# Kernel optimization log

Measured on AMD Instinct MI355X. Metric: run time of the kernel, lower is better.

The kernel has to match this reference:

```python
import jax, jax.numpy as jnp
import numpy as np

B, M, H = 4, 128, 1024      # docs, padded mentions per doc, LUKE-large hidden
NH, L = 16, 1024            # attention heads, seq_len
E = 64                      # padded entities per doc
R = 512                     # entity pairs per doc
EMB, BS, NC = 768, 64, 97   # embed_size, block_size, num_class


def setup_inputs() -> dict:
    key = jax.random.key(0)
    ks = jax.random.split(key, 12)
    inp = {
        "seq_lhs": jax.random.normal(ks[0], (B, L, H), jnp.float32),
        "ent_lhs": jax.random.normal(ks[1], (B, M, H), jnp.float32),
        "ent_to_seq_attn": jax.random.uniform(ks[2], (B, NH, M, L), jnp.float32),
        "entity_id_labels": jax.random.randint(ks[3], (B, M), 0, E),
        "hts": jax.random.randint(ks[4], (B, R, 2), 0, E),
        "Wh": jax.random.normal(ks[5], (2 * H, EMB), jnp.float32) * 0.02,
        "bh": jax.random.normal(ks[6], (EMB,), jnp.float32) * 0.02,
        "Wt": jax.random.normal(ks[7], (2 * H, EMB), jnp.float32) * 0.02,
        "bt": jax.random.normal(ks[8], (EMB,), jnp.float32) * 0.02,
        "Wb": jax.random.normal(ks[9], (EMB * BS, NC), jnp.float32) * 0.02,
        "bb": jax.random.normal(ks[10], (NC,), jnp.float32) * 0.02,
    }
    return inp


def reference(seq_lhs, ent_lhs, ent_to_seq_attn, entity_id_labels, hts,
              Wh, bh, Wt, bt, Wb, bb):
    # ---- mention -> entity pooling (segment logsumexp / segment mean) ----
    # global segment id per mention: doc_i * E + entity_label
    ids = (jnp.arange(B)[:, None] * E + entity_id_labels).reshape(-1)  # [B*M]
    m = ent_lhs.reshape(B * M, H)

    seg_max = jax.ops.segment_max(m, ids, num_segments=B * E)          # [B*E, H]
    seg_max = jnp.where(jnp.isfinite(seg_max), seg_max, 0.0)           # empty -> 0
    sumexp = jax.ops.segment_sum(jnp.exp(m - seg_max[ids]), ids, num_segments=B * E)
    cnt = jax.ops.segment_sum(jnp.ones((B * M,), m.dtype), ids, num_segments=B * E)  # [B*E]
    lse = seg_max + jnp.log(jnp.maximum(sumexp, 1e-30))
    ent_embeds = jnp.where(cnt[:, None] > 0, lse, 0.0).reshape(B, E, H)

    # mean of entity-to-seq attention over mentions of each entity
    a = ent_to_seq_attn.transpose(0, 2, 1, 3).reshape(B * M, NH, L)
    a_sum = jax.ops.segment_sum(a, ids, num_segments=B * E)            # [B*E, NH, L]
    ent_attn = (a_sum / jnp.maximum(cnt, 1.0)[:, None, None]).reshape(B, E, NH, L)

    # ---- gather head/tail entities for each pair ----
    h_idx, t_idx = hts[..., 0], hts[..., 1]                            # [B, R]
    hs = jnp.take_along_axis(ent_embeds, h_idx[..., None], axis=1)     # [B, R, H]
    ts = jnp.take_along_axis(ent_embeds, t_idx[..., None], axis=1)
    h_attn = jnp.take_along_axis(ent_attn, h_idx[..., None, None], axis=1)  # [B, R, NH, L]
    t_attn = jnp.take_along_axis(ent_attn, t_idx[..., None, None], axis=1)

    # ---- attn-weighted relation-context embedding ----
    ht_attn = (h_attn * t_attn).mean(axis=2)                           # [B, R, L]
    ht_attn = ht_attn / (ht_attn.sum(-1, keepdims=True) + 1e-5)
    rel = jnp.einsum('bld,brl->brd', seq_lhs, ht_attn)                 # [B, R, H]

    # ---- extractors + block bilinear classifier ----
    hs = jnp.tanh(jnp.concatenate([hs, rel], -1) @ Wh + bh)            # [B, R, EMB]
    ts = jnp.tanh(jnp.concatenate([ts, rel], -1) @ Wt + bt)
    N, K = B * R, EMB // BS
    b1 = hs.reshape(N, K, BS)
    b2 = ts.reshape(N, K, BS)
    bl = (b1[:, :, :, None] * b2[:, :, None, :]).reshape(N, EMB * BS)  # [N, 49152]
    class_logits = bl @ Wb + bb                                        # [N, NC]
    return class_logits
```

## Files before the change

### kernel.cpp

```cpp
#include <hip/hip_runtime.h>
#include <cmath>

#define B_ 4
#define M_ 128
#define H_ 1024
#define NH_ 16
#define L_ 1024
#define E_ 64
#define R_ 512
#define EMB_ 768
#define BS_ 64
#define NC_ 97
#define NPAIR_ (B_*R_)
#define LC_ 16

typedef _Float16 half8 __attribute__((ext_vector_type(8)));
typedef float f32x4 __attribute__((ext_vector_type(4)));

#define OFF_ENT    0
#define OFF_ATTNH  262144
#define OFF_VH     2359296
#define OFF_S      3407872
#define OFF_SEQT   3409920
#define OFF_RELH   5507072
#define OFF_HSF    6555648
#define OFF_TSF    7342080
#define OFF_WHT    8128512
#define OFF_WTT    8914944

__device__ __forceinline__ void gload_lds16(const void* g, void* l) {
    __builtin_amdgcn_global_load_lds(
        (const __attribute__((address_space(1))) unsigned int*)g,
        (__attribute__((address_space(3))) unsigned int*)l, 16, 0, 0);
}

__global__ __launch_bounds__(256) void k_ent_pool(const float* __restrict__ ent_lhs,
                                                  const int* __restrict__ labels,
                                                  float* __restrict__ ent_embeds) {
    int blk = blockIdx.x;
    int b = blk >> 6, e = blk & 63;
    __shared__ int lbl[M_];
    int t = threadIdx.x;
    if (t < M_) lbl[t] = labels[b*M_ + t];
    __syncthreads();
    const float* src = ent_lhs + (size_t)b * M_ * H_;
    float mx[4], sm[4];
    #pragma unroll
    for (int j = 0; j < 4; ++j) { mx[j] = -INFINITY; sm[j] = 0.f; }
    int cnt = 0;
    for (int m = 0; m < M_; ++m) {
        if (lbl[m] != e) continue;
        ++cnt;
        const float* row = src + m * H_;
        #pragma unroll
        for (int j = 0; j < 4; ++j) {
            float x = row[t + j*256];
            if (x > mx[j]) { sm[j] = sm[j] * __expf(mx[j] - x) + 1.f; mx[j] = x; }
            else           { sm[j] += __expf(x - mx[j]); }
        }
    }
    float* dst = ent_embeds + (size_t)blk * H_;
    #pragma unroll
    for (int j = 0; j < 4; ++j)
        dst[t + j*256] = (cnt > 0) ? (mx[j] + __logf(sm[j])) : 0.f;
}

__global__ __launch_bounds__(256) void k_ent_attn(const float* __restrict__ attn,
                                                  const int* __restrict__ labels,
                                                  _Float16* __restrict__ ea_t) {
    int blk = blockIdx.x;
    int b = blk >> 6, e = blk & 63;
    __shared__ int lbl[M_];
    int t = threadIdx.x;
    if (t < M_) lbl[t] = labels[b*M_ + t];
    __syncthreads();
    const float* src = attn + (size_t)b * NH_ * M_ * L_;
    float acc[16][4] = {};
    int cnt = 0;
    for (int m = 0; m < M_; ++m) {
        if (lbl[m] != e) continue;
        ++cnt;
        const float* mp = src + (size_t)m * L_ + t*4;
        #pragma unroll
        for (int nh = 0; nh < 16; ++nh) {
            float4 v = *(const float4*)(mp + (size_t)nh * M_ * L_);
            acc[nh][0] += v.x; acc[nh][1] += v.y; acc[nh][2] += v.z; acc[nh][3] += v.w;
        }
    }
    float inv = 1.f / fmaxf((float)cnt, 1.f);
    _Float16* dst = ea_t + (size_t)blk * L_ * 16;
    #pragma unroll
    for (int j = 0; j < 4; ++j) {
        int l = t*4 + j;
        half8 o0, o1;
        #pragma unroll
        for (int nh = 0; nh < 8; ++nh) { o0[nh] = (_Float16)(acc[nh][j]*inv); o1[nh] = (_Float16)(acc[nh+8][j]*inv); }
        *(half8*)(dst + (size_t)l*16)     = o0;
        *(half8*)(dst + (size_t)l*16 + 8) = o1;
    }
}

__global__ __launch_bounds__(256) void k_ht(const _Float16* __restrict__ ea_t,
                                            const int* __restrict__ hts,
                                            _Float16* __restrict__ vh) {
    int blk = blockIdx.x;
    int b = blk >> 6, lc = blk & 63;
    int l0 = lc * LC_;
    __shared__ _Float16 tile[64*256];
    int t = threadIdx.x;
    {
        int e = t >> 2, part = t & 3;
        const _Float16* src = ea_t + ((size_t)(b*64 + e)*L_ + l0) * 16;
        #pragma unroll
        for (int u = 0; u < 8; ++u) {
            int unit = part*8 + u;
            int l = unit >> 1, nhh = unit & 1;
            half8 v = *(const half8*)(src + l*16 + nhh*8);
            *(half8*)&tile[e*256 + ((l ^ (e & 15))*16) + nhh*8] = v;
        }
    }
    __syncthreads();
    const int* hp = hts + b * R_ * 2;
    #pragma unroll
    for (int pp = 0; pp < 2; ++pp) {
        int p = pp*256 + t;
        int he = hp[p*2], te = hp[p*2 + 1];
        const _Float16* ha = &tile[he*256];
        const _Float16* ta = &tile[te*256];
        float accl[LC_];
        #pragma unroll
        for (int l = 0; l < LC_; ++l) {
            half8 h0 = *(const half8*)&ha[((l ^ (he & 15))*16)];
            half8 h1 = *(const half8*)&ha[((l ^ (he & 15))*16) + 8];
            half8 t0 = *(const half8*)&ta[((l ^ (te & 15))*16)];
            half8 t1 = *(const half8*)&ta[((l ^ (te & 15))*16) + 8];
            float s = 0.f;
            #pragma unroll
            for (int q = 0; q < 8; ++q)
                s += (float)h0[q]*(float)t0[q] + (float)h1[q]*(float)t1[q];
            accl[l] = s;
        }
        half8 o0, o1;
        #pragma unroll
        for (int q = 0; q < 8; ++q) { o0[q] = (_Float16)accl[q]; o1[q] = (_Float16)accl[q+8]; }
        _Float16* dst = vh + (size_t)(b*R_ + p)*L_ + l0;
        *(half8*)dst = o0;
        *(half8*)(dst + 8) = o1;
    }
}

__global__ __launch_bounds__(256) void k_rowsum(const _Float16* __restrict__ vh,
                                                float* __restrict__ s) {
    int row = blockIdx.x*4 + (threadIdx.x >> 6);
    int lane = threadIdx.x & 63;
    const _Float16* r = vh + (size_t)row * L_;
    float acc = 0.f;
    #pragma unroll
    for (int u = 0; u < 2; ++u) {
        half8 v = *(const half8*)(r + (lane + u*64)*8);
        #pragma unroll
        for (int q = 0; q < 8; ++q) acc += (float)v[q];
    }
    #pragma unroll
    for (int off = 32; off > 0; off >>= 1) acc += __shfl_down(acc, off);
    if (lane == 0) s[row] = acc;
}

__global__ __launch_bounds__(256) void k_prep_seqt(const float* __restrict__ seq,
                                                   _Float16* __restrict__ seqT) {
    int l0 = blockIdx.x*64, d0 = blockIdx.y*64, b = blockIdx.z;
    __shared__ _Float16 sl[64*72];
    int t = threadIdx.x;
    int lr = t >> 4, dc = (t & 15)*4;
    #pragma unroll
    for (int u = 0; u < 4; ++u) {
        int l = lr + u*16;
        float4 v = *(const float4*)(seq + ((size_t)(b*L_ + l0 + l))*H_ + d0 + dc);
        sl[l*72 + dc+0] = (_Float16)v.x; sl[l*72 + dc+1] = (_Float16)v.y;
        sl[l*72 + dc+2] = (_Float16)v.z; sl[l*72 + dc+3] = (_Float16)v.w;
    }
    __syncthreads();
    int d = t >> 2, lo = (t & 3)*16;
    half8 o0, o1;
    #pragma unroll
    for (int q = 0; q < 8; ++q) { o0[q] = sl[(lo+q)*72 + d]; o1[q] = sl[(lo+8+q)*72 + d]; }
    _Float16* dst = seqT + ((size_t)(b*H_ + d0 + d))*L_ + l0 + lo;
    *(half8*)dst = o0;
    *(half8*)(dst + 8) = o1;
}

__global__ __launch_bounds__(256) void k_prep_wt(const float* __restrict__ W,
                                                 _Float16* __restrict__ WT) {
    int k0 = blockIdx.x * 64;
    int d0 = blockIdx.y * 64;
    __shared__ float s[64*65];
    int t = threadIdx.x;
    #pragma unroll
    for (int u = 0; u < 16; ++u) {
        int idx = t + u*256; int rr = idx >> 6, cc = idx & 63;
        s[rr*65 + cc] = W[(size_t)(k0+rr)*EMB_ + d0 + cc];
    }
    __syncthreads();
    #pragma unroll
    for (int u = 0; u < 16; ++u) {
        int idx = t + u*256; int dd = idx >> 6, kk = idx & 63;
        WT[(size_t)(d0+dd)*2048 + k0 + kk] = (_Float16)s[kk*65 + dd];
    }
}

__global__ __launch_bounds__(256) void k_prep_wbt(const float* __restrict__ Wb,
                                                  _Float16* __restrict__ Wbt) {
    int kbi = blockIdx.x;
    __shared__ float s[64*97];
    int t = threadIdx.x;
    size_t gbase = (size_t)kbi * 64 * NC_;
    #pragma unroll
    for (int u = 0; u < 25; ++u) {
        int idx = t + u*256;
        if (idx < 64*NC_) s[idx] = Wb[gbase + idx];
    }
    __syncthreads();
    _Float16* dst = Wbt + (size_t)kbi * 8192;
    #pragma unroll
    for (int u = 0; u < 32; ++u) {
        int idx = t + u*256;
        int c = idx >> 6, j = idx & 63;
        float v = (c < NC_) ? s[j*NC_ + c] : 0.f;
        dst[idx] = (_Float16)v;
    }
}

__global__ __launch_bounds__(256) void k_rel_mfma(const _Float16* __restrict__ vh,
                                                  const _Float16* __restrict__ seqT,
                                                  const float* __restrict__ s,
                                                  _Float16* __restrict__ relh) {
    const int d0 = blockIdx.x * 64;
    const int n0 = blockIdx.y * 64;
    const int b  = n0 >> 9;
    __shared__ _Float16 bs[2][64*64];
    const int t = threadIdx.x;
    const int w = t >> 6, lane = t & 63;
    const int r = lane & 15, g = lane >> 4;
    const int row8 = lane >> 3, u8 = lane & 7;
    const int swz_w = (u8 ^ row8) * 8;

    const _Float16* bsrc = seqT + ((size_t)(b*H_) + d0) * L_;
    #pragma unroll
    for (int c2 = w*2; c2 < w*2+2; ++c2)
        gload_lds16(bsrc + (size_t)(c2*8 + row8)*L_ + swz_w, &bs[0][c2*512]);

    const _Float16* ap = vh + (size_t)(n0 + w*16 + r) * L_;
    half8 nA0 = *(const half8*)(ap + g*8);
    half8 nA1 = *(const half8*)(ap + 32 + g*8);

    f32x4 acc[4] = {};
    __syncthreads();

    for (int c = 0; c < 16; ++c) {
        const int cur = c & 1;
        if (c < 15) {
            const int k0n = (c+1)*64;
            #pragma unroll
            for (int c2 = w*2; c2 < w*2+2; ++c2)
                gload_lds16(bsrc + (size_t)(c2*8 + row8)*L_ + k0n + swz_w, &bs[cur^1][c2*512]);
        }
        half8 cA0 = nA0, cA1 = nA1;
        if (c < 15) {
            const int k0n = (c+1)*64;
            nA0 = *(const half8*)(ap + k0n + g*8);
            nA1 = *(const half8*)(ap + k0n + 32 + g*8);
        }
        #pragma unroll
        for (int df = 0; df < 4; ++df) {
            half8 b0 = *(const half8*)&bs[cur][(df*16 + r)*64 + ((g ^ (r&7))*8)];
            acc[df] = __builtin_amdgcn_mfma_f32_16x16x32_f16(cA0, b0, acc[df], 0, 0, 0);
            half8 b1 = *(const half8*)&bs[cur][(df*16 + r)*64 + (((4+g) ^ (r&7))*8)];
            acc[df] = __builtin_amdgcn_mfma_f32_16x16x32_f16(cA1, b1, acc[df], 0, 0, 0);
        }
        __syncthreads();
    }
    const int nb = n0 + w*16 + g*4;
    float invs[4];
    #pragma unroll
    for (int q = 0; q < 4; ++q) invs[q] = 1.f / (s[nb + q] + 1.6e-4f);
    #pragma unroll
    for (int df = 0; df < 4; ++df)
        #pragma unroll
        for (int q = 0; q < 4; ++q)
            relh[(size_t)(nb + q)*H_ + d0 + df*16 + r] = (_Float16)(acc[df][q] * invs[q]);
}

__global__ __launch_bounds__(256) void k_extract_mfma(const float* __restrict__ ent_embeds,
                                                      const _Float16* __restrict__ relh,
                                                      const int* __restrict__ hts,
                                                      const _Float16* __restrict__ WhT,
                                                      const _Float16* __restrict__ WtT,
                                                      const float* __restrict__ bh,
                                                      const float* __restrict__ bt,
                                                      _Float16* __restrict__ hsf,
                                                      _Float16* __restrict__ tsf) {
    const int which = blockIdx.z;
    const _Float16* WT = which ? WtT : WhT;
    const float* bias  = which ? bt : bh;
    _Float16* outh     = which ? tsf : hsf;

    const int d0 = blockIdx.x * 64;
    const int n0 = blockIdx.y * 64;
    __shared__ _Float16 wt_s[2][64*64];
    const int t = threadIdx.x;
    const int w = t >> 6, lane = t & 63;
    const int r = lane & 15, g = lane >> 4;
    const int row8 = lane >> 3, u8 = lane & 7;
    const int swz_w = (u8 ^ row8) * 8;

    const int nrow = n0 + w*16 + r;
    const int hidx = hts[nrow*2 + which];
    const float* entp = ent_embeds + ((size_t)((nrow >> 9)*E_ + hidx))*H_;
    const _Float16* relp = relh + (size_t)nrow * H_;

    #pragma unroll
    for (int c2 = w*2; c2 < w*2+2; ++c2)
        gload_lds16(WT + (size_t)(d0 + c2*8 + row8)*2048 + swz_w, &wt_s[0][c2*512]);

    float4 nF0 = *(const float4*)(entp + g*8);
    float4 nF1 = *(const float4*)(entp + g*8 + 4);
    float4 nF2 = *(const float4*)(entp + 32 + g*8);
    float4 nF3 = *(const float4*)(entp + 32 + g*8 + 4);
    half8 nH0 = {}, nH1 = {};

    f32x4 acc[4] = {};
    __syncthreads();

    for (int c = 0; c < 32; ++c) {
        const int cur = c & 1;
        if (c < 31) {
            const int k0n = (c+1)*64;
            #pragma unroll
            for (int c2 = w*2; c2 < w*2+2; ++c2)
                gload_lds16(WT + (size_t)(d0 + c2*8 + row8)*2048 + k0n + swz_w,
                            &wt_s[cur^1][c2*512]);
        }
        half8 aF0, aF1;
        if (c < 16) {
            aF0 = half8{ (_Float16)nF0.x, (_Float16)nF0.y, (_Float16)nF0.z, (_Float16)nF0.w,
                         (_Float16)nF1.x, (_Float16)nF1.y, (_Float16)nF1.z, (_Float16)nF1.w };
            aF1 = half8{ (_Float16)nF2.x, (_Float16)nF2.y, (_Float16)nF2.z, (_Float16)nF2.w,
                         (_Float16)nF3.x, (_Float16)nF3.y, (_Float16)nF3.z, (_Float16)nF3.w };
        } else {
            aF0 = nH0; aF1 = nH1;
        }
        if (c < 31) {
            const int k0n = (c+1)*64;
            if (k0n < 1024) {
                const float* ar = entp + k0n;
                nF0 = *(const float4*)(ar + g*8);
                nF1 = *(const float4*)(ar + g*8 + 4);
                nF2 = *(const float4*)(ar + 32 + g*8);
                nF3 = *(const float4*)(ar + 32 + g*8 + 4);
            } else {
                const _Float16* ar = relp + (k0n - 1024);
                nH0 = *(const half8*)(ar + g*8);
                nH1 = *(const half8*)(ar + 32 + g*8);
            }
        }
        #pragma unroll
        for (int df = 0; df < 4; ++df) {
            half8 b0 = *(const half8*)&wt_s[cur][(df*16 + r)*64 + ((g ^ (r&7))*8)];
            acc[df] = __builtin_amdgcn_mfma_f32_16x16x32_f16(aF0, b0, acc[df], 0, 0, 0);
            half8 b1 = *(const half8*)&wt_s[cur][(df*16 + r)*64 + (((4+g) ^ (r&7))*8)];
            acc[df] = __builtin_amdgcn_mfma_f32_16x16x32_f16(aF1, b1, acc[df], 0, 0, 0);
        }
        __syncthreads();
    }
    #pragma unroll
    for (int df = 0; df < 4; ++df) {
        float bv = bias[d0 + df*16 + r];
        #pragma unroll
        for (int q2 = 0; q2 < 4; ++q2) {
            float v = tanhf(acc[df][q2] + bv);
            outh[(size_t)(n0 + w*16 + g*4 + q2)*EMB_ + d0 + df*16 + r] = (_Float16)v;
        }
    }
}

__global__ __launch_bounds__(256) void k_cls_mfma(const _Float16* __restrict__ hsf,
                                                  const _Float16* __restrict__ tsf,
                                                  const _Float16* __restrict__ Wbt,
                                                  float* __restrict__ partial) {
    const int kb = blockIdx.x;
    const int n0 = blockIdx.y * 128;
    const int t = threadIdx.x;
    const int w = t >> 6, lane = t & 63;
    const int r = lane & 15, g = lane >> 4;
    __shared__ _Float16 hs_s[128*72];

    {
        int n = t & 127, hh = t >> 7;
        const _Float16* src = &hsf[(size_t)(n0+n)*EMB_ + kb*64 + hh*32];
        #pragma unroll
        for (int u = 0; u < 4; ++u)
            *(half8*)&hs_s[n*72 + hh*32 + u*8] = *(const half8*)(src + u*8);
    }
    half8 tsF[8][2];
    #pragma unroll
    for (int nf = 0; nf < 8; ++nf) {
        const _Float16* tp = &tsf[(size_t)(n0 + nf*16 + r)*EMB_ + kb*64];
        tsF[nf][0] = *(const half8*)(tp + g*8);
        tsF[nf][1] = *(const half8*)(tp + 32 + g*8);
    }
    __syncthreads();

    const _Float16* wb = Wbt + (size_t)(kb*64) * 8192;
    f32x4 acc[8][2] = {};

    #pragma unroll 2
    for (int i = 0; i < 64; ++i) {
        const _Float16* ws_ = wb + (size_t)i * 8192;
        half8 b00, b01, b10, b11;
        {
            const _Float16* bp0 = ws_ + (size_t)(w*32 + r)*64;
            const _Float16* bp1 = ws_ + (size_t)(w*32 + 16 + r)*64;
            b00 = *(const half8*)(bp0 + g*8);
            b01 = *(const half8*)(bp0 + 32 + g*8);
            b10 = *(const half8*)(bp1 + g*8);
            b11 = *(const half8*)(bp1 + 32 + g*8);
        }
        #pragma unroll
        for (int nf = 0; nf < 8; ++nf) {
            _Float16 h = hs_s[(nf*16 + r)*72 + i];
            half8 a0, a1;
            #pragma unroll
            for (int e = 0; e < 8; ++e) { a0[e] = tsF[nf][0][e] * h; a1[e] = tsF[nf][1][e] * h; }
            acc[nf][0] = __builtin_amdgcn_mfma_f32_16x16x32_f16(a0, b00, acc[nf][0], 0, 0, 0);
            acc[nf][0] = __builtin_amdgcn_mfma_f32_16x16x32_f16(a1, b01, acc[nf][0], 0, 0, 0);
            acc[nf][1] = __builtin_amdgcn_mfma_f32_16x16x32_f16(a0, b10, acc[nf][1], 0, 0, 0);
            acc[nf][1] = __builtin_amdgcn_mfma_f32_16x16x32_f16(a1, b11, acc[nf][1], 0, 0, 0);
        }
    }
    float* pdst = partial + (size_t)kb * 2048 * 128;
    #pragma unroll
    for (int nf = 0; nf < 8; ++nf) {
        #pragma unroll
        for (int cl = 0; cl < 2; ++cl) {
            int c = w*32 + cl*16 + r;
            #pragma unroll
            for (int q = 0; q < 4; ++q)
                pdst[(size_t)(n0 + nf*16 + g*4 + q)*128 + c] = acc[nf][cl][q];
        }
    }
}

__global__ __launch_bounds__(256) void k_reduce(const float* __restrict__ partial,
                                                const float* __restrict__ bb,
                                                float* __restrict__ out) {
    int idx = blockIdx.x*256 + threadIdx.x;
    if (idx >= NPAIR_*NC_) return;
    int n = idx / NC_, c = idx - n*NC_;
    float s = bb[c];
    #pragma unroll
    for (int kb = 0; kb < 12; ++kb)
        s += partial[((size_t)kb*2048 + n)*128 + c];
    out[idx] = s;
}

extern "C" void kernel_launch(void* const* d_in, const int* in_sizes, int n_in,
                              void* d_out, int out_size, void* d_ws, size_t ws_size,
                              hipStream_t stream) {
    (void)in_sizes; (void)n_in; (void)out_size; (void)ws_size;
    const float* seq  = (const float*)d_in[0];
    const float* ent  = (const float*)d_in[1];
    const float* attn = (const float*)d_in[2];
    const int*   lbl  = (const int*)d_in[3];
    const int*   hts  = (const int*)d_in[4];
    const float* Wh   = (const float*)d_in[5];
    const float* bh   = (const float*)d_in[6];
    const float* Wt   = (const float*)d_in[7];
    const float* bt   = (const float*)d_in[8];
    const float* Wb   = (const float*)d_in[9];
    const float* bb   = (const float*)d_in[10];
    float* out = (float*)d_out;
    float* ws  = (float*)d_ws;

    float*    ent_embeds = ws + OFF_ENT;
    _Float16* ea_t = (_Float16*)(ws + OFF_ATTNH);
    _Float16* vh   = (_Float16*)(ws + OFF_VH);
    float*    sv   = ws + OFF_S;
    _Float16* seqT = (_Float16*)(ws + OFF_SEQT);
    _Float16* relh = (_Float16*)(ws + OFF_RELH);
    _Float16* hsf  = (_Float16*)(ws + OFF_HSF);
    _Float16* tsf  = (_Float16*)(ws + OFF_TSF);
    _Float16* WhT  = (_Float16*)(ws + OFF_WHT);
    _Float16* WtT  = (_Float16*)(ws + OFF_WTT);
    _Float16* Wbt  = (_Float16*)(ws + OFF_ATTNH);
    float*    part = ws + OFF_SEQT;

    k_prep_seqt<<<dim3(16, 16, 4), 256, 0, stream>>>(seq, seqT);
    k_prep_wt<<<dim3(32, 12), 256, 0, stream>>>(Wh, WhT);
    k_prep_wt<<<dim3(32, 12), 256, 0, stream>>>(Wt, WtT);
    k_ent_pool<<<B_*E_, 256, 0, stream>>>(ent, lbl, ent_embeds);
    k_ent_attn<<<B_*E_, 256, 0, stream>>>(attn, lbl, ea_t);
    k_ht<<<B_*64, 256, 0, stream>>>(ea_t, hts, vh);
    k_rowsum<<<NPAIR_/4, 256, 0, stream>>>(vh, sv);
    k_rel_mfma<<<dim3(16, 32), 256, 0, stream>>>(vh, seqT, sv, relh);
    k_prep_wbt<<<768, 256, 0, stream>>>(Wb, Wbt);
    k_extract_mfma<<<dim3(12, 32, 2), 256, 0, stream>>>(ent_embeds, relh, hts, WhT, WtT, bh, bt, hsf, tsf);
    k_cls_mfma<<<dim3(12, 16), 256, 0, stream>>>(hsf, tsf, Wbt, part);
    k_reduce<<<(NPAIR_*NC_ + 255)/256, 256, 0, stream>>>(part, bb, out);
}
```

Measured before the change: 292.6 us.

## Split extractor GEMM into per-entity and per-pair parts and enlarge MFMA tiles

The concat([ent, rel]) @ W product is split algebraically. The entity half is computed once per unique entity (256 rows) instead of once per pair, and the relation half is computed per pair. Both halves for Wh and Wt go through one larger 128x128-tile MFMA GEMM into an fp16 buffer G. A small combine kernel then gathers by hts, adds the bias and applies tanh. The rel GEMM also moves to 128x64 tiles with both operands staged in LDS, and the workspace layout is reshuffled. This removes redundant FLOPs on the entity half, at the cost of an extra fp16 rounding of partial sums and one extra kernel launch.

Result: faster. 281.2 us (-3.9%).

```diff
diff --git a/kernel.cpp b/kernel.cpp
--- a/kernel.cpp
+++ b/kernel.cpp
@@ -17,16 +17,17 @@
 typedef _Float16 half8 __attribute__((ext_vector_type(8)));
 typedef float f32x4 __attribute__((ext_vector_type(4)));
 
-#define OFF_ENT    0
-#define OFF_ATTNH  262144
-#define OFF_VH     2359296
-#define OFF_S      3407872
-#define OFF_SEQT   3409920
-#define OFF_RELH   5507072
-#define OFF_HSF    6555648
-#define OFF_TSF    7342080
-#define OFF_WHT    8128512
-#define OFF_WTT    8914944
+#define OFF_EAT    0
+#define OFF_VH     2097152
+#define OFF_PART   0
+#define OFF_SEQT   3145728
+#define OFF_G      3145728
+#define OFF_RELH   5242880
+#define OFF_WBT    6291456
+#define OFF_ENTH   9437184
+#define OFF_SV     9568256
+#define OFF_WHT    9570304
+#define OFF_WTT    10356736
 
 __device__ __forceinline__ void gload_lds16(const void* g, void* l) {
     __builtin_amdgcn_global_load_lds(
@@ -36,7 +37,7 @@
 
 __global__ __launch_bounds__(256) void k_ent_pool(const float* __restrict__ ent_lhs,
                                                   const int* __restrict__ labels,
-                                                  float* __restrict__ ent_embeds) {
+                                                  _Float16* __restrict__ enth) {
     int blk = blockIdx.x;
     int b = blk >> 6, e = blk & 63;
     __shared__ int lbl[M_];
@@ -59,10 +60,10 @@
             else           { sm[j] += __expf(x - mx[j]); }
         }
     }
-    float* dst = ent_embeds + (size_t)blk * H_;
+    _Float16* dst = enth + (size_t)blk * H_;
     #pragma unroll
     for (int j = 0; j < 4; ++j)
-        dst[t + j*256] = (cnt > 0) ? (mx[j] + __logf(sm[j])) : 0.f;
+        dst[t + j*256] = (_Float16)((cnt > 0) ? (mx[j] + __logf(sm[j])) : 0.f);
 }
 
 __global__ __launch_bounds__(256) void k_ent_attn(const float* __restrict__ attn,
@@ -230,157 +231,181 @@
     }
 }
 
-__global__ __launch_bounds__(256) void k_rel_mfma(const _Float16* __restrict__ vh,
-                                                  const _Float16* __restrict__ seqT,
-                                                  const float* __restrict__ s,
-                                                  _Float16* __restrict__ relh) {
-    const int d0 = blockIdx.x * 64;
-    const int n0 = blockIdx.y * 64;
-    const int b  = n0 >> 9;
-    __shared__ _Float16 bs[2][64*64];
+__global__ __launch_bounds__(256) void k_relmm(const _Float16* __restrict__ vh,
+                                               const _Float16* __restrict__ seqT,
+                                               const float* __restrict__ sv,
+                                               _Float16* __restrict__ relh) {
+    const int nt = blockIdx.x;
+    const int mt = blockIdx.y;
+    const int b  = mt >> 2;
+    __shared__ _Float16 As[2][128*64];
+    __shared__ _Float16 Bs[2][64*64];
     const int t = threadIdx.x;
     const int w = t >> 6, lane = t & 63;
     const int r = lane & 15, g = lane >> 4;
-    const int row8 = lane >> 3, u8 = lane & 7;
-    const int swz_w = (u8 ^ row8) * 8;
-
-    const _Float16* bsrc = seqT + ((size_t)(b*H_) + d0) * L_;
-    #pragma unroll
-    for (int c2 = w*2; c2 < w*2+2; ++c2)
-        gload_lds16(bsrc + (size_t)(c2*8 + row8)*L_ + swz_w, &bs[0][c2*512]);
-
-    const _Float16* ap = vh + (size_t)(n0 + w*16 + r) * L_;
-    half8 nA0 = *(const half8*)(ap + g*8);
-    half8 nA1 = *(const half8*)(ap + 32 + g*8);
-
-    f32x4 acc[4] = {};
-    __syncthreads();
-
-    for (int c = 0; c < 16; ++c) {
-        const int cur = c & 1;
-        if (c < 15) {
-            const int k0n = (c+1)*64;
-            #pragma unroll
-            for (int c2 = w*2; c2 < w*2+2; ++c2)
-                gload_lds16(bsrc + (size_t)(c2*8 + row8)*L_ + k0n + swz_w, &bs[cur^1][c2*512]);
-        }
-        half8 cA0 = nA0, cA1 = nA1;
-        if (c < 15) {
-            const int k0n = (c+1)*64;
-            nA0 = *(const half8*)(ap + k0n + g*8);
-            nA1 = *(const half8*)(ap + k0n + 32 + g*8);
-        }
-        #pragma unroll
-        for (int df = 0; df < 4; ++df) {
-            half8 b0 = *(const half8*)&bs[cur][(df*16 + r)*64 + ((g ^ (r&7))*8)];
-            acc[df] = __builtin_amdgcn_mfma_f32_16x16x32_f16(cA0, b0, acc[df], 0, 0, 0);
-            half8 b1 = *(const half8*)&bs[cur][(df*16 + r)*64 + (((4+g) ^ (r&7))*8)];
-            acc[df] = __builtin_amdgcn_mfma_f32_16x16x32_f16(cA1, b1, acc[df], 0, 0, 0);
-        }
+    const int wm = w >> 1, wn = w & 1;
+    const int srow = lane >> 3, scol = ((lane & 7) ^ srow) * 8;
+
+    const _Float16* Ab = vh + (size_t)mt*128*1024;
+    const _Float16* Bb = seqT + ((size_t)b*1024 + nt*64)*1024;
+
+    #pragma unroll
+    for (int cc = 0; cc < 6; ++cc) {
+        int c = w*6 + cc;
+        if (c < 16) gload_lds16(Ab + (size_t)(c*8 + srow)*1024 + scol, &As[0][c*512]);
+        else        gload_lds16(Bb + (size_t)((c-16)*8 + srow)*1024 + scol, &Bs[0][(c-16)*512]);
+    }
+    f32x4 acc[4][2] = {};
+    __syncthreads();
+
+    for (int k = 0; k < 16; ++k) {
+        const int cur = k & 1;
+        if (k < 15) {
+            const int k0 = (k+1)*64;
+            #pragma unroll
+            for (int cc = 0; cc < 6; ++cc) {
+                int c = w*6 + cc;
+                if (c < 16) gload_lds16(Ab + (size_t)(c*8 + srow)*1024 + k0 + scol, &As[cur^1][c*512]);
+                else        gload_lds16(Bb + (size_t)((c-16)*8 + srow)*1024 + k0 + scol, &Bs[cur^1][(c-16)*512]);
+            }
+        }
+        half8 aF[4][2], bF[2][2];
+        #pragma unroll
+        for (int mf = 0; mf < 4; ++mf) {
+            int row = wm*64 + mf*16 + r;
+            aF[mf][0] = *(const half8*)&As[cur][row*64 + ((g ^ (r&7))*8)];
+            aF[mf][1] = *(const half8*)&As[cur][row*64 + (((4+g) ^ (r&7))*8)];
+        }
+        #pragma unroll
+        for (int nf = 0; nf < 2; ++nf) {
+            int row = wn*32 + nf*16 + r;
+            bF[nf][0] = *(const half8*)&Bs[cur][row*64 + ((g ^ (r&7))*8)];
+            bF[nf][1] = *(const half8*)&Bs[cur][row*64 + (((4+g) ^ (r&7))*8)];
+        }
+        #pragma unroll
+        for (int mf = 0; mf < 4; ++mf)
+            #pragma unroll
+            for (int nf = 0; nf < 2; ++nf) {
+                acc[mf][nf] = __builtin_amdgcn_mfma_f32_16x16x32_f16(aF[mf][0], bF[nf][0], acc[mf][nf], 0, 0, 0);
+                acc[mf][nf] = __builtin_amdgcn_mfma_f32_16x16x32_f16(aF[mf][1], bF[nf][1], acc[mf][nf], 0, 0, 0);
+            }
         __syncthreads();
     }
-    const int nb = n0 + w*16 + g*4;
-    float invs[4];
-    #pragma unroll
-    for (int q = 0; q < 4; ++q) invs[q] = 1.f / (s[nb + q] + 1.6e-4f);
-    #pragma unroll
-    for (int df = 0; df < 4; ++df)
-        #pragma unroll
-        for (int q = 0; q < 4; ++q)
-            relh[(size_t)(nb + q)*H_ + d0 + df*16 + r] = (_Float16)(acc[df][q] * invs[q]);
-}
-
-__global__ __launch_bounds__(256) void k_extract_mfma(const float* __restrict__ ent_embeds,
-                                                      const _Float16* __restrict__ relh,
-                                                      const int* __restrict__ hts,
-                                                      const _Float16* __restrict__ WhT,
-                                                      const _Float16* __restrict__ WtT,
-                                                      const float* __restrict__ bh,
-                                                      const float* __restrict__ bt,
-                                                      _Float16* __restrict__ hsf,
-                                                      _Float16* __restrict__ tsf) {
-    const int which = blockIdx.z;
-    const _Float16* WT = which ? WtT : WhT;
-    const float* bias  = which ? bt : bh;
-    _Float16* outh     = which ? tsf : hsf;
-
-    const int d0 = blockIdx.x * 64;
-    const int n0 = blockIdx.y * 64;
-    __shared__ _Float16 wt_s[2][64*64];
+    #pragma unroll
+    for (int mf = 0; mf < 4; ++mf) {
+        int nb = mt*128 + wm*64 + mf*16 + g*4;
+        float invs[4];
+        #pragma unroll
+        for (int q = 0; q < 4; ++q) invs[q] = 1.f / (sv[nb + q] + 1.6e-4f);
+        #pragma unroll
+        for (int nf = 0; nf < 2; ++nf) {
+            int d = nt*64 + wn*32 + nf*16 + r;
+            #pragma unroll
+            for (int q = 0; q < 4; ++q)
+                relh[(size_t)(nb + q)*1024 + d] = (_Float16)(acc[mf][nf][q] * invs[q]);
+        }
+    }
+}
+
+__global__ __launch_bounds__(256) void k_bigmm(const _Float16* __restrict__ relh,
+                                               const _Float16* __restrict__ enth,
+                                               const _Float16* __restrict__ WhT,
+                                               const _Float16* __restrict__ WtT,
+                                               _Float16* __restrict__ G) {
+    const int nt = blockIdx.x;
+    const int mt = blockIdx.y;
+    __shared__ _Float16 As[2][128*64];
+    __shared__ _Float16 Bs[2][128*64];
     const int t = threadIdx.x;
     const int w = t >> 6, lane = t & 63;
     const int r = lane & 15, g = lane >> 4;
-    const int row8 = lane >> 3, u8 = lane & 7;
-    const int swz_w = (u8 ^ row8) * 8;
-
-    const int nrow = n0 + w*16 + r;
-    const int hidx = hts[nrow*2 + which];
-    const float* entp = ent_embeds + ((size_t)((nrow >> 9)*E_ + hidx))*H_;
-    const _Float16* relp = relh + (size_t)nrow * H_;
-
-    #pragma unroll
-    for (int c2 = w*2; c2 < w*2+2; ++c2)
-        gload_lds16(WT + (size_t)(d0 + c2*8 + row8)*2048 + swz_w, &wt_s[0][c2*512]);
-
-    float4 nF0 = *(const float4*)(entp + g*8);
-    float4 nF1 = *(const float4*)(entp + g*8 + 4);
-    float4 nF2 = *(const float4*)(entp + 32 + g*8);
-    float4 nF3 = *(const float4*)(entp + 32 + g*8 + 4);
-    half8 nH0 = {}, nH1 = {};
-
-    f32x4 acc[4] = {};
-    __syncthreads();
-
-    for (int c = 0; c < 32; ++c) {
-        const int cur = c & 1;
-        if (c < 31) {
-            const int k0n = (c+1)*64;
-            #pragma unroll
-            for (int c2 = w*2; c2 < w*2+2; ++c2)
-                gload_lds16(WT + (size_t)(d0 + c2*8 + row8)*2048 + k0n + swz_w,
-                            &wt_s[cur^1][c2*512]);
-        }
-        half8 aF0, aF1;
-        if (c < 16) {
-            aF0 = half8{ (_Float16)nF0.x, (_Float16)nF0.y, (_Float16)nF0.z, (_Float16)nF0.w,
-                         (_Float16)nF1.x, (_Float16)nF1.y, (_Float16)nF1.z, (_Float16)nF1.w };
-            aF1 = half8{ (_Float16)nF2.x, (_Float16)nF2.y, (_Float16)nF2.z, (_Float16)nF2.w,
-                         (_Float16)nF3.x, (_Float16)nF3.y, (_Float16)nF3.z, (_Float16)nF3.w };
-        } else {
-            aF0 = nH0; aF1 = nH1;
-        }
-        if (c < 31) {
-            const int k0n = (c+1)*64;
-            if (k0n < 1024) {
-                const float* ar = entp + k0n;
-                nF0 = *(const float4*)(ar + g*8);
-                nF1 = *(const float4*)(ar + g*8 + 4);
-                nF2 = *(const float4*)(ar + 32 + g*8);
-                nF3 = *(const float4*)(ar + 32 + g*8 + 4);
-            } else {
-                const _Float16* ar = relp + (k0n - 1024);
-                nH0 = *(const half8*)(ar + g*8);
-                nH1 = *(const half8*)(ar + 32 + g*8);
+    const int wm = w >> 1, wn = w & 1;
+    const int srow = lane >> 3, scol = ((lane & 7) ^ srow) * 8;
+
+    const _Float16* Ab = (mt < 16) ? (relh + (size_t)mt*128*1024)
+                                   : (enth + (size_t)(mt-16)*128*1024);
+    const int koff = (mt < 16) ? 1024 : 0;
+    const _Float16* Bb = ((nt < 6) ? (WhT + (size_t)nt*128*2048)
+                                   : (WtT + (size_t)(nt-6)*128*2048)) + koff;
+
+    #pragma unroll
+    for (int cc = 0; cc < 4; ++cc) {
+        int c = w*4 + cc;
+        gload_lds16(Ab + (size_t)(c*8 + srow)*1024 + scol, &As[0][c*512]);
+        gload_lds16(Bb + (size_t)(c*8 + srow)*2048 + scol, &Bs[0][c*512]);
+    }
+    f32x4 acc[4][4] = {};
+    __syncthreads();
+
+    for (int k = 0; k < 16; ++k) {
+        const int cur = k & 1;
+        if (k < 15) {
+            const int k0 = (k+1)*64;
+            #pragma unroll
+            for (int cc = 0; cc < 4; ++cc) {
+                int c = w*4 + cc;
+                gload_lds16(Ab + (size_t)(c*8 + srow)*1024 + k0 + scol, &As[cur^1][c*512]);
+                gload_lds16(Bb + (size_t)(c*8 + srow)*2048 + k0 + scol, &Bs[cur^1][c*512]);
             }
         }
-        #pragma unroll
-        for (int df = 0; df < 4; ++df) {
-            half8 b0 = *(const half8*)&wt_s[cur][(df*16 + r)*64 + ((g ^ (r&7))*8)];
-            acc[df] = __builtin_amdgcn_mfma_f32_16x16x32_f16(aF0, b0, acc[df], 0, 0, 0);
-            half8 b1 = *(const half8*)&wt_s[cur][(df*16 + r)*64 + (((4+g) ^ (r&7))*8)];
-            acc[df] = __builtin_amdgcn_mfma_f32_16x16x32_f16(aF1, b1, acc[df], 0, 0, 0);
-        }
+        half8 aF[4][2], bF[4][2];
+        #pragma unroll
+        for (int mf = 0; mf < 4; ++mf) {
+            int row = wm*64 + mf*16 + r;
+            aF[mf][0] = *(const half8*)&As[cur][row*64 + ((g ^ (r&7))*8)];
+            aF[mf][1] = *(const half8*)&As[cur][row*64 + (((4+g) ^ (r&7))*8)];
+        }
+        #pragma unroll
+        for (int nf = 0; nf < 4; ++nf) {
+            int row = wn*64 + nf*16 + r;
+            bF[nf][0] = *(const half8*)&Bs[cur][row*64 + ((g ^ (r&7))*8)];
+            bF[nf][1] = *(const half8*)&Bs[cur][row*64 + (((4+g) ^ (r&7))*8)];
+        }
+        #pragma unroll
+        for (int mf = 0; mf < 4; ++mf)
+            #pragma unroll
+            for (int nf = 0; nf < 4; ++nf) {
+                acc[mf][nf] = __builtin_amdgcn_mfma_f32_16x16x32_f16(aF[mf][0], bF[nf][0], acc[mf][nf], 0, 0, 0);
+                acc[mf][nf] = __builtin_amdgcn_mfma_f32_16x16x32_f16(aF[mf][1], bF[nf][1], acc[mf][nf], 0, 0, 0);
+            }
         __syncthreads();
     }
     #pragma unroll
-    for (int df = 0; df < 4; ++df) {
-        float bv = bias[d0 + df*16 + r];
-        #pragma unroll
-        for (int q2 = 0; q2 < 4; ++q2) {
-            float v = tanhf(acc[df][q2] + bv);
-            outh[(size_t)(n0 + w*16 + g*4 + q2)*EMB_ + d0 + df*16 + r] = (_Float16)v;
-        }
-    }
+    for (int mf = 0; mf < 4; ++mf) {
+        int nrow = mt*128 + wm*64 + mf*16 + g*4;
+        #pragma unroll
+        for (int nf = 0; nf < 4; ++nf) {
+            int v = nt*128 + wn*64 + nf*16 + r;
+            #pragma unroll
+            for (int q = 0; q < 4; ++q)
+                G[(size_t)(nrow + q)*1536 + v] = (_Float16)acc[mf][nf][q];
+        }
+    }
+}
+
+__global__ __launch_bounds__(192) void k_combine(const _Float16* __restrict__ G,
+                                                 const int* __restrict__ hts,
+                                                 const float* __restrict__ bh,
+                                                 const float* __restrict__ bt,
+                                                 _Float16* __restrict__ hsf,
+                                                 _Float16* __restrict__ tsf) {
+    int n = blockIdx.x;
+    int b = n >> 9;
+    int t = threadIdx.x;
+    int side = t / 96, u = t % 96;
+    int d0 = u*8;
+    int idx = hts[n*2 + side];
+    const _Float16* grel = G + (size_t)n*1536 + side*768 + d0;
+    const _Float16* gent = G + (size_t)(2048 + b*64 + idx)*1536 + side*768 + d0;
+    const float* bias = side ? bt : bh;
+    half8 a = *(const half8*)grel;
+    half8 e = *(const half8*)gent;
+    half8 o;
+    #pragma unroll
+    for (int q = 0; q < 8; ++q)
+        o[q] = (_Float16)tanhf((float)a[q] + (float)e[q] + bias[d0+q]);
+    _Float16* dst = (side ? tsf : hsf) + (size_t)n*EMB_ + d0;
+    *(half8*)dst = o;
 }
 
 __global__ __launch_bounds__(256) void k_cls_mfma(const _Float16* __restrict__ hsf,
@@ -481,29 +506,31 @@
     float* out = (float*)d_out;
     float* ws  = (float*)d_ws;
 
-    float*    ent_embeds = ws + OFF_ENT;
-    _Float16* ea_t = (_Float16*)(ws + OFF_ATTNH);
+    _Float16* ea_t = (_Float16*)(ws + OFF_EAT);
     _Float16* vh   = (_Float16*)(ws + OFF_VH);
-    float*    sv   = ws + OFF_S;
+    float*    part = ws + OFF_PART;
     _Float16* seqT = (_Float16*)(ws + OFF_SEQT);
+    _Float16* G    = (_Float16*)(ws + OFF_G);
     _Float16* relh = (_Float16*)(ws + OFF_RELH);
-    _Float16* hsf  = (_Float16*)(ws + OFF_HSF);
-    _Float16* tsf  = (_Float16*)(ws + OFF_TSF);
+    _Float16* Wbt  = (_Float16*)(ws + OFF_WBT);
+    _Float16* enth = (_Float16*)(ws + OFF_ENTH);
+    float*    sv   = ws + OFF_SV;
     _Float16* WhT  = (_Float16*)(ws + OFF_WHT);
     _Float16* WtT  = (_Float16*)(ws + OFF_WTT);
-    _Float16* Wbt  = (_Float16*)(ws + OFF_ATTNH);
-    float*    part = ws + OFF_SEQT;
+    _Float16* hsf  = (_Float16*)(ws + OFF_WHT);
+    _Float16* tsf  = (_Float16*)(ws + OFF_WTT);
 
     k_prep_seqt<<<dim3(16, 16, 4), 256, 0, stream>>>(seq, seqT);
     k_prep_wt<<<dim3(32, 12), 256, 0, stream>>>(Wh, WhT);
     k_prep_wt<<<dim3(32, 12), 256, 0, stream>>>(Wt, WtT);
-    k_ent_pool<<<B_*E_, 256, 0, stream>>>(ent, lbl, ent_embeds);
+    k_prep_wbt<<<768, 256, 0, stream>>>(Wb, Wbt);
+    k_ent_pool<<<B_*E_, 256, 0, stream>>>(ent, lbl, enth);
     k_ent_attn<<<B_*E_, 256, 0, stream>>>(attn, lbl, ea_t);
     k_ht<<<B_*64, 256, 0, stream>>>(ea_t, hts, vh);
     k_rowsum<<<NPAIR_/4, 256, 0, stream>>>(vh, sv);
-    k_rel_mfma<<<dim3(16, 32), 256, 0, stream>>>(vh, seqT, sv, relh);
-    k_prep_wbt<<<768, 256, 0, stream>>>(Wb, Wbt);
-    k_extract_mfma<<<dim3(12, 32, 2), 256, 0, stream>>>(ent_embeds, relh, hts, WhT, WtT, bh, bt, hsf, tsf);
+    k_relmm<<<dim3(16, 16), 256, 0, stream>>>(vh, seqT, sv, relh);
+    k_bigmm<<<dim3(12, 18), 256, 0, stream>>>(relh, enth, WhT, WtT, G);
+    k_combine<<<NPAIR_, 192, 0, stream>>>(G, hts, bh, bt, hsf, tsf);
     k_cls_mfma<<<dim3(12, 16), 256, 0, stream>>>(hsf, tsf, Wbt, part);
     k_reduce<<<(NPAIR_*NC_ + 255)/256, 256, 0, stream>>>(part, bb, out);
 }
```
